# Optimization experiments

Hardware: AMD Instinct MI355X
Metric: run time of the kernel (lower is better)

The kernel has to match this reference:

```python
import jax, jax.numpy as jnp
import numpy as np


def _attention(q, k, v):
    # q: [B, Nq, C], k/v: [B, Nk, C]; scale by C**-0.5 as in the torch module
    C = q.shape[-1]
    scores = jnp.einsum('bqc,bkc->bqk', q, k) * (C ** -0.5)
    attn = jax.nn.softmax(scores, axis=-1)
    return jnp.einsum('bqk,bkc->bqc', attn, v)


def setup_inputs() -> dict:
    key = jax.random.key(0)
    ks = jax.random.split(key, 7)
    B, S, C, NL = 8192, 16, 256, 8
    return {
        'l1': jax.random.normal(ks[0], (B, S, C), dtype=jnp.float32),
        'a1': jax.random.normal(ks[1], (B, S, C), dtype=jnp.float32),
        'v1': jax.random.normal(ks[2], (B, S, C), dtype=jnp.float32),
        'latents': jax.random.normal(ks[3], (1, NL, C), dtype=jnp.float32) * 0.02,
        'scale_l': jax.random.normal(ks[4], (1,), dtype=jnp.float32) * 0.1,
        'scale_a': jax.random.normal(ks[5], (1,), dtype=jnp.float32) * 0.1,
        'scale_v': jax.random.normal(ks[6], (1,), dtype=jnp.float32) * 0.1,
    }


def reference(l1, a1, v1, latents, scale_l, scale_a, scale_v):
    B = l1.shape[0]
    lat = jnp.broadcast_to(latents, (B, latents.shape[1], latents.shape[2]))
    # 3 fixed fusion iterations (loop over layers, not data dims)
    for _ in range(3):
        concat_avt = jnp.concatenate((l1, a1, v1), axis=1)  # [B, 3S, C]
        fused = _attention(lat, concat_avt, concat_avt)      # [B, NL, C]
        l1 = l1 + scale_l * _attention(l1, fused, fused)
        a1 = a1 + scale_a * _attention(a1, fused, fused)
        v1 = v1 + scale_v * _attention(v1, fused, fused)
    # S > 1, so the original takes the last time-step
    return l1[:, -1, :]
```

## Files before the change

kernel.cpp:

```cpp
#include <hip/hip_runtime.h>
#include <math.h>

namespace {

constexpr int SEQ   = 16;
constexpr int CDIM  = 256;
constexpr int NLAT  = 8;
constexpr int NR    = 48;
constexpr int STRIDE = 260;

__device__ __forceinline__ float reduce8x16(const float acc[8], int id) {
    float p4[4];
    #pragma unroll
    for (int q = 0; q < 4; ++q) {
        const float a = acc[2*q]   + __shfl_xor(acc[2*q],   1);
        const float b = acc[2*q+1] + __shfl_xor(acc[2*q+1], 1);
        p4[q] = (id & 1) ? b : a;
    }
    float p2[2];
    #pragma unroll
    for (int q = 0; q < 2; ++q) {
        const float a = p4[2*q]   + __shfl_xor(p4[2*q],   2);
        const float b = p4[2*q+1] + __shfl_xor(p4[2*q+1], 2);
        p2[q] = (id & 2) ? b : a;
    }
    const float a = p2[0] + __shfl_xor(p2[0], 4);
    const float b = p2[1] + __shfl_xor(p2[1], 4);
    float r = (id & 4) ? b : a;
    r += __shfl_xor(r, 8);
    return r;
}

__global__ __launch_bounds__(256, 2)
void bottleneck_fusion_kernel(const float* __restrict__ l1,
                              const float* __restrict__ a1,
                              const float* __restrict__ v1,
                              const float* __restrict__ lat,
                              const float* __restrict__ psl,
                              const float* __restrict__ psa,
                              const float* __restrict__ psv,
                              float* __restrict__ out)
{
    __shared__ __align__(16) float st[NR * STRIDE];
    __shared__ __align__(16) float fz[NLAT * STRIDE];
    __shared__ __align__(16) float latl[NLAT * STRIDE];
    __shared__ __align__(16) float s1t[NR * NLAT];
    __shared__ __align__(16) float s2t[NR * NLAT];

    const int t    = threadIdx.x;
    const int wave = t >> 6;
    const int lane = t & 63;
    const int cg   = lane & 15;
    const int rs   = lane >> 4;
    const int b    = blockIdx.x;

    for (int idx = t; idx < NR * 64; idx += 256) {
        const int r = idx >> 6, c4 = idx & 63;
        const float* src = (r < 16) ? l1 : (r < 32) ? a1 : v1;
        const int row = r & 15;
        *(float4*)&st[r * STRIDE + c4 * 4] =
            *(const float4*)(src + ((size_t)b * SEQ + row) * CDIM + c4 * 4);
    }
    for (int idx = t; idx < NLAT * 64; idx += 256) {
        const int q = idx >> 6, c4 = idx & 63;
        float4 lv = *(const float4*)(lat + q * CDIM + c4 * 4);
        lv.x *= 0.0625f; lv.y *= 0.0625f; lv.z *= 0.0625f; lv.w *= 0.0625f;
        *(float4*)&latl[q * STRIDE + c4 * 4] = lv;
    }
    const float sc_l = psl[0], sc_a = psa[0], sc_v = psv[0];
    __syncthreads();

    for (int it = 0; it < 3; ++it) {
        {
            float latf[NLAT][16];
            #pragma unroll
            for (int q = 0; q < NLAT; ++q)
                #pragma unroll
                for (int h = 0; h < 4; ++h) {
                    const float4 lv = *(const float4*)&latl[q * STRIDE + h * 64 + cg * 4];
                    latf[q][h*4+0] = lv.x; latf[q][h*4+1] = lv.y;
                    latf[q][h*4+2] = lv.z; latf[q][h*4+3] = lv.w;
                }
            #pragma unroll
            for (int g = 0; g < 3; ++g) {
                const int r = wave * 12 + g * 4 + rs;
                float x[16];
                #pragma unroll
                for (int h = 0; h < 4; ++h) {
                    const float4 xv = *(const float4*)&st[r * STRIDE + h * 64 + cg * 4];
                    x[h*4+0] = xv.x; x[h*4+1] = xv.y; x[h*4+2] = xv.z; x[h*4+3] = xv.w;
                }
                float acc[NLAT];
                #pragma unroll
                for (int q = 0; q < NLAT; ++q) {
                    float s = 0.f;
                    #pragma unroll
                    for (int c = 0; c < 16; ++c) s = fmaf(x[c], latf[q][c], s);
                    acc[q] = s;
                }
                const float wv = reduce8x16(acc, cg);
                if (cg < NLAT) s1t[r * NLAT + cg] = wv;
            }
        }
        __syncthreads();

        {
            const int q = wave * 2 + (lane >> 5);
            const int j = lane & 31;
            const float va = s1t[j * NLAT + q];
            const float vb = (j < 16) ? s1t[(32 + j) * NLAT + q] : -1e30f;
            float m = fmaxf(va, vb);
            #pragma unroll
            for (int s = 1; s <= 16; s <<= 1) m = fmaxf(m, __shfl_xor(m, s));
            const float ea = __expf(va - m);
            const float eb = (j < 16) ? __expf(vb - m) : 0.f;
            float ssum = ea + eb;
            #pragma unroll
            for (int s = 1; s <= 16; s <<= 1) ssum += __shfl_xor(ssum, s);
            const float inv = 1.f / ssum;
            s1t[j * NLAT + q] = ea * inv;
            if (j < 16) s1t[(32 + j) * NLAT + q] = eb * inv;
        }
        __syncthreads();

        {
            float f[NLAT] = {0,0,0,0,0,0,0,0};
            #pragma unroll 4
            for (int k = 0; k < NR; ++k) {
                const float x = st[k * STRIDE + t];
                const float4 wa = *(const float4*)&s1t[k * NLAT];
                const float4 wb = *(const float4*)&s1t[k * NLAT + 4];
                f[0] = fmaf(wa.x, x, f[0]); f[1] = fmaf(wa.y, x, f[1]);
                f[2] = fmaf(wa.z, x, f[2]); f[3] = fmaf(wa.w, x, f[3]);
                f[4] = fmaf(wb.x, x, f[4]); f[5] = fmaf(wb.y, x, f[5]);
                f[6] = fmaf(wb.z, x, f[6]); f[7] = fmaf(wb.w, x, f[7]);
            }
            #pragma unroll
            for (int q = 0; q < NLAT; ++q) fz[q * STRIDE + t] = f[q];
        }
        __syncthreads();

        if (it < 2 || wave == 1) {
            float ff[NLAT][16];
            #pragma unroll
            for (int q = 0; q < NLAT; ++q)
                #pragma unroll
                for (int h = 0; h < 4; ++h) {
                    const float4 fv = *(const float4*)&fz[q * STRIDE + h * 64 + cg * 4];
                    ff[q][h*4+0] = fv.x; ff[q][h*4+1] = fv.y;
                    ff[q][h*4+2] = fv.z; ff[q][h*4+3] = fv.w;
                }
            #pragma unroll
            for (int g = 0; g < 3; ++g) {
                if (it == 2 && g != 0) continue;
                const int r = wave * 12 + g * 4 + rs;
                float x[16];
                #pragma unroll
                for (int h = 0; h < 4; ++h) {
                    const float4 xv = *(const float4*)&st[r * STRIDE + h * 64 + cg * 4];
                    x[h*4+0] = xv.x; x[h*4+1] = xv.y; x[h*4+2] = xv.z; x[h*4+3] = xv.w;
                }
                float acc[NLAT];
                #pragma unroll
                for (int q = 0; q < NLAT; ++q) {
                    float s = 0.f;
                    #pragma unroll
                    for (int c = 0; c < 16; ++c) s = fmaf(x[c], ff[q][c], s);
                    acc[q] = s * 0.0625f;
                }
                const float wv = reduce8x16(acc, cg);
                if (cg < NLAT) s2t[r * NLAT + cg] = wv;
            }
        }
        __syncthreads();

        {
            for (int r = (t >> 3); r < NR; r += 32) {
                const float v = s2t[r * NLAT + (t & 7)];
                float m = v;
                #pragma unroll
                for (int s = 1; s <= 4; s <<= 1) m = fmaxf(m, __shfl_xor(m, s));
                const float e = __expf(v - m);
                float ssum = e;
                #pragma unroll
                for (int s = 1; s <= 4; s <<= 1) ssum += __shfl_xor(ssum, s);
                s2t[r * NLAT + (t & 7)] = e / ssum;
            }
        }
        __syncthreads();

        if (it < 2 || wave == 1) {
            float f2[NLAT][4];
            #pragma unroll
            for (int j = 0; j < NLAT; ++j) {
                const float4 fv = *(const float4*)&fz[j * STRIDE + lane * 4];
                f2[j][0] = fv.x; f2[j][1] = fv.y; f2[j][2] = fv.z; f2[j][3] = fv.w;
            }
            for (int rr = 0; rr < 12; ++rr) {
                const int r = wave * 12 + rr;
                if (it == 2 && r != 15) continue;
                float w[NLAT];
                #pragma unroll
                for (int j = 0; j < NLAT; ++j) w[j] = s2t[r * NLAT + j];
                float4 xv = *(float4*)&st[r * STRIDE + lane * 4];
                float o0 = 0, o1 = 0, o2 = 0, o3 = 0;
                #pragma unroll
                for (int j = 0; j < NLAT; ++j) {
                    o0 = fmaf(w[j], f2[j][0], o0);
                    o1 = fmaf(w[j], f2[j][1], o1);
                    o2 = fmaf(w[j], f2[j][2], o2);
                    o3 = fmaf(w[j], f2[j][3], o3);
                }
                const float sc = (r < 16) ? sc_l : (r < 32) ? sc_a : sc_v;
                xv.x = fmaf(sc, o0, xv.x); xv.y = fmaf(sc, o1, xv.y);
                xv.z = fmaf(sc, o2, xv.z); xv.w = fmaf(sc, o3, xv.w);
                *(float4*)&st[r * STRIDE + lane * 4] = xv;
            }
        }
        __syncthreads();
    }

    if (t < 64) {
        *(float4*)(out + (size_t)b * CDIM + t * 4) = *(const float4*)&st[15 * STRIDE + t * 4];
    }
}

}

extern "C" void kernel_launch(void* const* d_in, const int* in_sizes, int n_in,
                              void* d_out, int out_size, void* d_ws, size_t ws_size,
                              hipStream_t stream) {
    const float* l1  = (const float*)d_in[0];
    const float* a1  = (const float*)d_in[1];
    const float* v1  = (const float*)d_in[2];
    const float* lat = (const float*)d_in[3];
    const float* psl = (const float*)d_in[4];
    const float* psa = (const float*)d_in[5];
    const float* psv = (const float*)d_in[6];
    float* out = (float*)d_out;

    const int B = in_sizes[0] / (SEQ * CDIM);
    dim3 grid(B), block(256);
    hipLaunchKernelGGL(bottleneck_fusion_kernel, grid, block, 0, stream,
                       l1, a1, v1, lat, psl, psa, psv, out);
}
```

Measured before the change: 743.7 us.

## Use 512-thread blocks, fuse second softmax and update into one stage

Doubles the block to 512 threads, with each 32-lane group owning 3 rows and reducing over 8 contiguous columns per lane. The second-stage scores, softmax and residual update are fused into one register-resident pass, which drops the s2t buffer and two block-wide barriers per iteration. The padded row stride is removed, which may reintroduce LDS bank conflicts. The larger block also raises the launch bound and register-pressure constraints.

```diff
diff --git a/kernel.cpp b/kernel.cpp
--- a/kernel.cpp
+++ b/kernel.cpp
@@ -3,35 +3,35 @@
 
 namespace {
 
-constexpr int SEQ   = 16;
-constexpr int CDIM  = 256;
-constexpr int NLAT  = 8;
-constexpr int NR    = 48;
-constexpr int STRIDE = 260;
-
-__device__ __forceinline__ float reduce8x16(const float acc[8], int id) {
+constexpr int SEQ  = 16;
+constexpr int CDIM = 256;
+constexpr int NLAT = 8;
+constexpr int NR   = 48;
+
+__device__ __forceinline__ float reduce32x8(const float acc[8], int ln) {
     float p4[4];
     #pragma unroll
-    for (int q = 0; q < 4; ++q) {
-        const float a = acc[2*q]   + __shfl_xor(acc[2*q],   1);
-        const float b = acc[2*q+1] + __shfl_xor(acc[2*q+1], 1);
-        p4[q] = (id & 1) ? b : a;
+    for (int i = 0; i < 4; ++i) {
+        const float a  = acc[2*i]   + __shfl_xor(acc[2*i],   1);
+        const float bq = acc[2*i+1] + __shfl_xor(acc[2*i+1], 1);
+        p4[i] = (ln & 1) ? bq : a;
     }
     float p2[2];
     #pragma unroll
-    for (int q = 0; q < 2; ++q) {
-        const float a = p4[2*q]   + __shfl_xor(p4[2*q],   2);
-        const float b = p4[2*q+1] + __shfl_xor(p4[2*q+1], 2);
-        p2[q] = (id & 2) ? b : a;
-    }
-    const float a = p2[0] + __shfl_xor(p2[0], 4);
-    const float b = p2[1] + __shfl_xor(p2[1], 4);
-    float r = (id & 4) ? b : a;
+    for (int i = 0; i < 2; ++i) {
+        const float a  = p4[2*i]   + __shfl_xor(p4[2*i],   2);
+        const float bq = p4[2*i+1] + __shfl_xor(p4[2*i+1], 2);
+        p2[i] = (ln & 2) ? bq : a;
+    }
+    const float a  = p2[0] + __shfl_xor(p2[0], 4);
+    const float bq = p2[1] + __shfl_xor(p2[1], 4);
+    float r = (ln & 4) ? bq : a;
     r += __shfl_xor(r, 8);
+    r += __shfl_xor(r, 16);
     return r;
 }
 
-__global__ __launch_bounds__(256, 2)
+__global__ __launch_bounds__(512, 4)
 void bottleneck_fusion_kernel(const float* __restrict__ l1,
                               const float* __restrict__ a1,
                               const float* __restrict__ v1,
@@ -41,187 +41,148 @@
                               const float* __restrict__ psv,
                               float* __restrict__ out)
 {
-    __shared__ __align__(16) float st[NR * STRIDE];
-    __shared__ __align__(16) float fz[NLAT * STRIDE];
-    __shared__ __align__(16) float latl[NLAT * STRIDE];
+    __shared__ __align__(16) float st[NR * CDIM];
+    __shared__ __align__(16) float fz[NLAT * CDIM];
+    __shared__ __align__(16) float latl[NLAT * CDIM];
     __shared__ __align__(16) float s1t[NR * NLAT];
-    __shared__ __align__(16) float s2t[NR * NLAT];
-
-    const int t    = threadIdx.x;
-    const int wave = t >> 6;
-    const int lane = t & 63;
-    const int cg   = lane & 15;
-    const int rs   = lane >> 4;
-    const int b    = blockIdx.x;
-
-    for (int idx = t; idx < NR * 64; idx += 256) {
-        const int r = idx >> 6, c4 = idx & 63;
+
+    const int t   = threadIdx.x;
+    const int wv  = t >> 6;
+    const int ln  = t & 63;
+    const int g   = t >> 5;
+    const int l32 = t & 31;
+    const int b   = blockIdx.x;
+
+    for (int idx = t; idx < NR * 64; idx += 512) {
+        const int r = idx >> 6, c4 = (idx & 63) * 4;
         const float* src = (r < 16) ? l1 : (r < 32) ? a1 : v1;
-        const int row = r & 15;
-        *(float4*)&st[r * STRIDE + c4 * 4] =
-            *(const float4*)(src + ((size_t)b * SEQ + row) * CDIM + c4 * 4);
-    }
-    for (int idx = t; idx < NLAT * 64; idx += 256) {
-        const int q = idx >> 6, c4 = idx & 63;
-        float4 lv = *(const float4*)(lat + q * CDIM + c4 * 4);
+        *(float4*)&st[r * CDIM + c4] =
+            *(const float4*)(src + ((size_t)b * SEQ + (r & 15)) * CDIM + c4);
+    }
+    {
+        const int q = t >> 6, c4 = (t & 63) * 4;
+        float4 lv = *(const float4*)(lat + q * CDIM + c4);
         lv.x *= 0.0625f; lv.y *= 0.0625f; lv.z *= 0.0625f; lv.w *= 0.0625f;
-        *(float4*)&latl[q * STRIDE + c4 * 4] = lv;
+        *(float4*)&latl[q * CDIM + c4] = lv;
     }
     const float sc_l = psl[0], sc_a = psa[0], sc_v = psv[0];
     __syncthreads();
 
     for (int it = 0; it < 3; ++it) {
         {
-            float latf[NLAT][16];
-            #pragma unroll
-            for (int q = 0; q < NLAT; ++q)
-                #pragma unroll
-                for (int h = 0; h < 4; ++h) {
-                    const float4 lv = *(const float4*)&latl[q * STRIDE + h * 64 + cg * 4];
-                    latf[q][h*4+0] = lv.x; latf[q][h*4+1] = lv.y;
-                    latf[q][h*4+2] = lv.z; latf[q][h*4+3] = lv.w;
-                }
-            #pragma unroll
-            for (int g = 0; g < 3; ++g) {
-                const int r = wave * 12 + g * 4 + rs;
-                float x[16];
-                #pragma unroll
-                for (int h = 0; h < 4; ++h) {
-                    const float4 xv = *(const float4*)&st[r * STRIDE + h * 64 + cg * 4];
-                    x[h*4+0] = xv.x; x[h*4+1] = xv.y; x[h*4+2] = xv.z; x[h*4+3] = xv.w;
-                }
+            float lf[NLAT][8];
+            #pragma unroll
+            for (int q = 0; q < NLAT; ++q) {
+                *(float4*)&lf[q][0] = *(const float4*)&latl[q * CDIM + l32 * 8];
+                *(float4*)&lf[q][4] = *(const float4*)&latl[q * CDIM + l32 * 8 + 4];
+            }
+            #pragma unroll
+            for (int rr = 0; rr < 3; ++rr) {
+                const int r = g * 3 + rr;
+                float x[8];
+                *(float4*)&x[0] = *(const float4*)&st[r * CDIM + l32 * 8];
+                *(float4*)&x[4] = *(const float4*)&st[r * CDIM + l32 * 8 + 4];
                 float acc[NLAT];
                 #pragma unroll
                 for (int q = 0; q < NLAT; ++q) {
                     float s = 0.f;
                     #pragma unroll
-                    for (int c = 0; c < 16; ++c) s = fmaf(x[c], latf[q][c], s);
+                    for (int c = 0; c < 8; ++c) s = fmaf(x[c], lf[q][c], s);
                     acc[q] = s;
                 }
-                const float wv = reduce8x16(acc, cg);
-                if (cg < NLAT) s1t[r * NLAT + cg] = wv;
+                const float s = reduce32x8(acc, l32);
+                if (l32 < NLAT) s1t[r * NLAT + l32] = s;
             }
         }
         __syncthreads();
 
         {
-            const int q = wave * 2 + (lane >> 5);
-            const int j = lane & 31;
-            const float va = s1t[j * NLAT + q];
-            const float vb = (j < 16) ? s1t[(32 + j) * NLAT + q] : -1e30f;
-            float m = fmaxf(va, vb);
-            #pragma unroll
-            for (int s = 1; s <= 16; s <<= 1) m = fmaxf(m, __shfl_xor(m, s));
-            const float ea = __expf(va - m);
-            const float eb = (j < 16) ? __expf(vb - m) : 0.f;
-            float ssum = ea + eb;
-            #pragma unroll
-            for (int s = 1; s <= 16; s <<= 1) ssum += __shfl_xor(ssum, s);
-            const float inv = 1.f / ssum;
-            s1t[j * NLAT + q] = ea * inv;
-            if (j < 16) s1t[(32 + j) * NLAT + q] = eb * inv;
+            const int q = wv, k = ln;
+            const bool act = (k < NR);
+            const float v = act ? s1t[k * NLAT + q] : -3.4e38f;
+            float m = v;
+            #pragma unroll
+            for (int d = 1; d <= 32; d <<= 1) m = fmaxf(m, __shfl_xor(m, d));
+            const float e = act ? __expf(v - m) : 0.f;
+            float ssum = e;
+            #pragma unroll
+            for (int d = 1; d <= 32; d <<= 1) ssum += __shfl_xor(ssum, d);
+            if (act) s1t[k * NLAT + q] = e / ssum;
         }
         __syncthreads();
 
         {
-            float f[NLAT] = {0,0,0,0,0,0,0,0};
+            const int c = t & 255, nib = t >> 8;
+            float f0 = 0.f, f1 = 0.f, f2 = 0.f, f3 = 0.f;
             #pragma unroll 4
             for (int k = 0; k < NR; ++k) {
-                const float x = st[k * STRIDE + t];
-                const float4 wa = *(const float4*)&s1t[k * NLAT];
-                const float4 wb = *(const float4*)&s1t[k * NLAT + 4];
-                f[0] = fmaf(wa.x, x, f[0]); f[1] = fmaf(wa.y, x, f[1]);
-                f[2] = fmaf(wa.z, x, f[2]); f[3] = fmaf(wa.w, x, f[3]);
-                f[4] = fmaf(wb.x, x, f[4]); f[5] = fmaf(wb.y, x, f[5]);
-                f[6] = fmaf(wb.z, x, f[6]); f[7] = fmaf(wb.w, x, f[7]);
-            }
-            #pragma unroll
-            for (int q = 0; q < NLAT; ++q) fz[q * STRIDE + t] = f[q];
-        }
-        __syncthreads();
-
-        if (it < 2 || wave == 1) {
-            float ff[NLAT][16];
-            #pragma unroll
-            for (int q = 0; q < NLAT; ++q)
-                #pragma unroll
-                for (int h = 0; h < 4; ++h) {
-                    const float4 fv = *(const float4*)&fz[q * STRIDE + h * 64 + cg * 4];
-                    ff[q][h*4+0] = fv.x; ff[q][h*4+1] = fv.y;
-                    ff[q][h*4+2] = fv.z; ff[q][h*4+3] = fv.w;
-                }
-            #pragma unroll
-            for (int g = 0; g < 3; ++g) {
-                if (it == 2 && g != 0) continue;
-                const int r = wave * 12 + g * 4 + rs;
-                float x[16];
-                #pragma unroll
-                for (int h = 0; h < 4; ++h) {
-                    const float4 xv = *(const float4*)&st[r * STRIDE + h * 64 + cg * 4];
-                    x[h*4+0] = xv.x; x[h*4+1] = xv.y; x[h*4+2] = xv.z; x[h*4+3] = xv.w;
-                }
+                const float4 w4 = *(const float4*)&s1t[k * NLAT + nib * 4];
+                const float xv = st[k * CDIM + c];
+                f0 = fmaf(w4.x, xv, f0);
+                f1 = fmaf(w4.y, xv, f1);
+                f2 = fmaf(w4.z, xv, f2);
+                f3 = fmaf(w4.w, xv, f3);
+            }
+            fz[(nib * 4 + 0) * CDIM + c] = f0;
+            fz[(nib * 4 + 1) * CDIM + c] = f1;
+            fz[(nib * 4 + 2) * CDIM + c] = f2;
+            fz[(nib * 4 + 3) * CDIM + c] = f3;
+        }
+        __syncthreads();
+
+        if (it < 2 || g == 5) {
+            float ff[NLAT][8];
+            #pragma unroll
+            for (int j = 0; j < NLAT; ++j) {
+                *(float4*)&ff[j][0] = *(const float4*)&fz[j * CDIM + l32 * 8];
+                *(float4*)&ff[j][4] = *(const float4*)&fz[j * CDIM + l32 * 8 + 4];
+            }
+            #pragma unroll
+            for (int rr = 0; rr < 3; ++rr) {
+                const int r = g * 3 + rr;
+                float x[8];
+                *(float4*)&x[0] = *(const float4*)&st[r * CDIM + l32 * 8];
+                *(float4*)&x[4] = *(const float4*)&st[r * CDIM + l32 * 8 + 4];
                 float acc[NLAT];
                 #pragma unroll
-                for (int q = 0; q < NLAT; ++q) {
+                for (int j = 0; j < NLAT; ++j) {
                     float s = 0.f;
                     #pragma unroll
-                    for (int c = 0; c < 16; ++c) s = fmaf(x[c], ff[q][c], s);
-                    acc[q] = s * 0.0625f;
+                    for (int c = 0; c < 8; ++c) s = fmaf(x[c], ff[j][c], s);
+                    acc[j] = s;
                 }
-                const float wv = reduce8x16(acc, cg);
-                if (cg < NLAT) s2t[r * NLAT + cg] = wv;
-            }
-        }
-        __syncthreads();
-
-        {
-            for (int r = (t >> 3); r < NR; r += 32) {
-                const float v = s2t[r * NLAT + (t & 7)];
-                float m = v;
-                #pragma unroll
-                for (int s = 1; s <= 4; s <<= 1) m = fmaxf(m, __shfl_xor(m, s));
-                const float e = __expf(v - m);
+                const float s = reduce32x8(acc, l32) * 0.0625f;
+                float m = s;
+                m = fmaxf(m, __shfl_xor(m, 1));
+                m = fmaxf(m, __shfl_xor(m, 2));
+                m = fmaxf(m, __shfl_xor(m, 4));
+                const float e = __expf(s - m);
                 float ssum = e;
-                #pragma unroll
-                for (int s = 1; s <= 4; s <<= 1) ssum += __shfl_xor(ssum, s);
-                s2t[r * NLAT + (t & 7)] = e / ssum;
-            }
-        }
-        __syncthreads();
-
-        if (it < 2 || wave == 1) {
-            float f2[NLAT][4];
-            #pragma unroll
-            for (int j = 0; j < NLAT; ++j) {
-                const float4 fv = *(const float4*)&fz[j * STRIDE + lane * 4];
-                f2[j][0] = fv.x; f2[j][1] = fv.y; f2[j][2] = fv.z; f2[j][3] = fv.w;
-            }
-            for (int rr = 0; rr < 12; ++rr) {
-                const int r = wave * 12 + rr;
-                if (it == 2 && r != 15) continue;
-                float w[NLAT];
-                #pragma unroll
-                for (int j = 0; j < NLAT; ++j) w[j] = s2t[r * NLAT + j];
-                float4 xv = *(float4*)&st[r * STRIDE + lane * 4];
-                float o0 = 0, o1 = 0, o2 = 0, o3 = 0;
+                ssum += __shfl_xor(ssum, 1);
+                ssum += __shfl_xor(ssum, 2);
+                ssum += __shfl_xor(ssum, 4);
+                const float wq = e / ssum;
+                float o[8] = {0,0,0,0,0,0,0,0};
+                const int obase = ln & ~7;
                 #pragma unroll
                 for (int j = 0; j < NLAT; ++j) {
-                    o0 = fmaf(w[j], f2[j][0], o0);
-                    o1 = fmaf(w[j], f2[j][1], o1);
-                    o2 = fmaf(w[j], f2[j][2], o2);
-                    o3 = fmaf(w[j], f2[j][3], o3);
+                    const float wj = __shfl(wq, obase | j);
+                    #pragma unroll
+                    for (int c = 0; c < 8; ++c) o[c] = fmaf(wj, ff[j][c], o[c]);
                 }
                 const float sc = (r < 16) ? sc_l : (r < 32) ? sc_a : sc_v;
-                xv.x = fmaf(sc, o0, xv.x); xv.y = fmaf(sc, o1, xv.y);
-                xv.z = fmaf(sc, o2, xv.z); xv.w = fmaf(sc, o3, xv.w);
-                *(float4*)&st[r * STRIDE + lane * 4] = xv;
+                #pragma unroll
+                for (int c = 0; c < 8; ++c) x[c] = fmaf(sc, o[c], x[c]);
+                *(float4*)&st[r * CDIM + l32 * 8]     = *(float4*)&x[0];
+                *(float4*)&st[r * CDIM + l32 * 8 + 4] = *(float4*)&x[4];
             }
         }
         __syncthreads();
     }
 
     if (t < 64) {
-        *(float4*)(out + (size_t)b * CDIM + t * 4) = *(const float4*)&st[15 * STRIDE + t * 4];
+        *(float4*)(out + (size_t)b * CDIM + t * 4) =
+            *(const float4*)&st[15 * CDIM + t * 4];
     }
 }
 
@@ -240,7 +201,7 @@
     float* out = (float*)d_out;
 
     const int B = in_sizes[0] / (SEQ * CDIM);
-    dim3 grid(B), block(256);
+    dim3 grid(B), block(512);
     hipLaunchKernelGGL(bottleneck_fusion_kernel, grid, block, 0, stream,
                        l1, a1, v1, lat, psl, psa, psv, out);
 }
```

After: 799.2 us. 1.07x slower.
